# Kernel tuning notes

Hardware: AMD Instinct MI355X
Metric: run time of the kernel (lower is better)

## Reference

```python
import jax, jax.numpy as jnp
import numpy as np

B, G, IN, OUT, H, W = 8, 3, 384, 384, 64, 64
CG, OG = IN // G, OUT // G  # channels per group


def setup_inputs() -> dict:
    key = jax.random.key(0)
    ks = jax.random.split(key, 6)
    return {
        "input": jax.random.normal(ks[0], (B, IN, H, W), jnp.float32),
        "wh_pred": jax.random.uniform(ks[1], (B, 2 * G, H, W), jnp.float32),
        # conv_offset: 1x1 grouped conv, groups=G, in=2 per group, out=18 per group
        "w_off": jax.random.normal(ks[2], (G, 18, 2), jnp.float32) * 0.1,
        "b_off": jax.random.normal(ks[3], (G, 18), jnp.float32) * 0.1,
        # deformable 3x3 conv, groups=G: weight [OUT, IN/G, 3, 3]
        "w_d": jax.random.normal(ks[4], (OUT, CG, 3, 3), jnp.float32) * (1.0 / np.sqrt(CG * 9)),
        "b_d": jax.random.normal(ks[5], (OUT,), jnp.float32) * 0.01,
    }


def _bilinear_sample(img, py, px):
    # img: [Cg, H, W]; py, px: [9, H, W] float sampling positions
    # zero padding outside bounds (torchvision deform_conv2d semantics)
    y0 = jnp.floor(py)
    x0 = jnp.floor(px)
    wy = py - y0  # weight toward y0+1
    wx = px - x0
    y0i = y0.astype(jnp.int32)
    x0i = x0.astype(jnp.int32)

    def gather(yi, xi):
        valid = (yi >= 0) & (yi < H) & (xi >= 0) & (xi < W)
        yc = jnp.clip(yi, 0, H - 1)
        xc = jnp.clip(xi, 0, W - 1)
        v = img[:, yc, xc]  # [Cg, 9, H, W]
        return v * valid[None].astype(img.dtype)

    v00 = gather(y0i, x0i)
    v01 = gather(y0i, x0i + 1)
    v10 = gather(y0i + 1, x0i)
    v11 = gather(y0i + 1, x0i + 1)
    return (v00 * ((1 - wy) * (1 - wx))[None]
            + v01 * ((1 - wy) * wx)[None]
            + v10 * (wy * (1 - wx))[None]
            + v11 * (wy * wx)[None])  # [Cg, 9, H, W]


def _forward(input, wh_pred, w_off, b_off, w_d, b_d):
    # conv_offset: grouped 1x1 conv on detached wh_pred
    wh = jax.lax.stop_gradient(wh_pred).reshape(B, G, 2, H, W)
    off = jnp.einsum('bgchw,goc->bgohw', wh, w_off) + b_off[None, :, :, None, None]
    off = off.reshape(B, G, 9, 2, H, W)  # (dy, dx) per kernel tap

    # sampling positions for 3x3 kernel, stride 1, pad 1
    ky = (jnp.arange(9) // 3 - 1).astype(jnp.float32)
    kx = (jnp.arange(9) % 3 - 1).astype(jnp.float32)
    hh = jnp.arange(H, dtype=jnp.float32)
    ww = jnp.arange(W, dtype=jnp.float32)
    py = off[:, :, :, 0] + hh[None, None, None, :, None] + ky[None, None, :, None, None]
    px = off[:, :, :, 1] + ww[None, None, None, None, :] + kx[None, None, :, None, None]

    xg = input.reshape(B, G, CG, H, W)
    samp = jax.vmap(jax.vmap(_bilinear_sample))(xg, py, px)  # [B, G, Cg, 9, H, W]

    wg = w_d.reshape(G, OG, CG, 9)
    out = jnp.einsum('bgckhw,gock->bgohw', samp, wg)
    out = out.reshape(B, OUT, H, W) + b_d[None, :, None, None]
    return out


def reference(input, wh_pred, w_off, b_off, w_d, b_d):
    return _forward(input, wh_pred, w_off, b_off, w_d, b_d)
```

## Files before the change

kernel.cpp:

```cpp
#include <hip/hip_runtime.h>


typedef __attribute__((ext_vector_type(8))) short short8;
typedef __attribute__((ext_vector_type(4))) float floatx4;
typedef __attribute__((ext_vector_type(4))) unsigned int uintx4;

#define SLAB 524288
#define XT_GUARD 8704
#define XT_TAIL 512

__device__ __forceinline__ float bf_lo(unsigned int d) {
  return __uint_as_float(d << 16);
}
__device__ __forceinline__ float bf_hi(unsigned int d) {
  return __uint_as_float(d & 0xffff0000u);
}
__device__ __forceinline__ unsigned int cvtpk_bf16(float lo, float hi) {
  unsigned int r;
  asm("v_cvt_pk_bf16_f32 %0, %1, %2" : "=v"(r) : "v"(lo), "v"(hi));
  return r;
}

__global__ __launch_bounds__(256) void transpose_x_kernel(
    const float* __restrict__ in, ushort* __restrict__ xT) {
  __shared__ float tile[32][33];
  const int t  = threadIdx.x;
  const int tx = t & 31, ty = t >> 5;
  const int bx = blockIdx.x;
  const int x0 = (bx & 1) * 32;
  const int c0 = (bx >> 1) * 32;
  const int y  = blockIdx.y;
  const int bg = blockIdx.z;
  const int b  = bg / 3, g = bg % 3;

  const float* src = in + ((size_t)(b * 384 + g * 128)) * 4096 + (size_t)y * 64;
#pragma unroll
  for (int it = 0; it < 4; ++it) {
    int c = c0 + ty + it * 8;
    tile[ty + it * 8][tx] = src[(size_t)c * 4096 + x0 + tx];
  }
  __syncthreads();
  ushort* dst = xT + (((size_t)bg * 64 + y) * 64) * 128;
#pragma unroll
  for (int it = 0; it < 4; ++it) {
    int x = x0 + ty + it * 8;
    float v = tile[tx][ty + it * 8];
    dst[(size_t)x * 128 + c0 + tx] =
        (ushort)((__float_as_uint(v) + 0x8000u) >> 16);
  }
}

__global__ __launch_bounds__(256) void swizzle_w_kernel(
    const float* __restrict__ w_d, ushort* __restrict__ wB) {
  int idx = blockIdx.x * 256 + threadIdx.x;
  if (idx >= 442368) return;
  int j  = idx & 7;
  int l  = (idx >> 3) & 63;
  int f  = (idx >> 9) & 7;
  int s  = (idx >> 12) & 3;
  int t2 = idx >> 14;
  int k  = t2 % 9;
  int g  = t2 / 9;
  int o  = f * 16 + (l & 15);
  int c  = s * 32 + (l >> 4) * 8 + j;
  float v = w_d[((size_t)(g * 128 + o) * 128 + c) * 9 + k];
  wB[idx] = (ushort)((__float_as_uint(v) + 0x8000u) >> 16);
}

__global__ __launch_bounds__(256) void fa_main_mfma(
    const ushort* __restrict__ xT, const ushort* __restrict__ wB,
    const float* __restrict__ wh_pred, const float* __restrict__ w_off,
    const float* __restrict__ b_off, const float* __restrict__ b_d,
    float* __restrict__ out) {
  __shared__ int    off_s[9][32];
  __shared__ float4 w4_s[9][32];
  __shared__ ushort samp[32][128];

  const int t   = threadIdx.x;
  const int bid = blockIdx.x;
  const int b   = bid & 7;
  const int rem = bid >> 3;
  const int ph  = rem & 1;
  const int h   = (rem >> 1) & 63;
  const int g   = rem >> 7;
  const int pos0 = ph * 32;

  for (int idx = t; idx < 288; idx += 256) {
    int k = idx >> 5, pos = idx & 31;
    int posg = pos0 + pos;
    float wh0 = wh_pred[(((size_t)b * 6 + g * 2 + 0) * 64 + h) * 64 + posg];
    float wh1 = wh_pred[(((size_t)b * 6 + g * 2 + 1) * 64 + h) * 64 + posg];
    int oy_i = g * 18 + k * 2;
    int ox_i = oy_i + 1;
    float oy = fmaf(w_off[oy_i * 2], wh0, fmaf(w_off[oy_i * 2 + 1], wh1, b_off[oy_i]));
    float ox = fmaf(w_off[ox_i * 2], wh0, fmaf(w_off[ox_i * 2 + 1], wh1, b_off[ox_i]));
    float py = oy + (float)(h + k / 3 - 1);
    float px = ox + (float)(posg + k % 3 - 1);

    float fy = floorf(py), fx = floorf(px);
    int y0 = (int)fy, x0 = (int)fx;
    float wy = py - fy, wx = px - fx;
    float m_y0 = ((unsigned)y0 < 64u) ? 1.f : 0.f;
    float m_y1 = ((unsigned)(y0 + 1) < 64u) ? 1.f : 0.f;
    float m_x0 = ((unsigned)x0 < 64u) ? 1.f : 0.f;
    float m_x1 = ((unsigned)(x0 + 1) < 64u) ? 1.f : 0.f;
    float4 w4;
    w4.x = (1.f - wy) * (1.f - wx) * m_y0 * m_x0;
    w4.y = (1.f - wy) * wx * m_y0 * m_x1;
    w4.z = wy * (1.f - wx) * m_y1 * m_x0;
    w4.w = wy * wx * m_y1 * m_x1;
    int y0c = min(max(y0, -1), 63);
    int x0c = min(max(x0, -1), 63);
    off_s[k][pos] = (y0c * 64 + x0c) * 128;
    w4_s[k][pos]  = w4;
  }
  __syncthreads();

  const int wv  = t >> 6;
  const int l   = t & 63;
  const int l15 = l & 15;
  const int lhi = l >> 4;

  floatx4 acc[2][2];
#pragma unroll
  for (int ia = 0; ia < 2; ++ia) {
#pragma unroll
    for (int r = 0; r < 4; ++r) {
      float bias = b_d[g * 128 + wv * 32 + ia * 16 + lhi * 4 + r];
#pragma unroll
      for (int jb = 0; jb < 2; ++jb) acc[ia][jb][r] = bias;
    }
  }

  const int spos = t >> 3;
  const int scq  = t & 7;
  const int swz  = (spos & 7) << 3;
  const ushort* xb = xT + (size_t)(b * 3 + g) * SLAB;
  const ushort* wg = wB + (size_t)g * 9 * 16384;

  for (int k = 0; k < 9; ++k) {
    {
      int off   = off_s[k][spos];
      float4 w4 = w4_s[k][spos];
      const ushort* p00 = xb + off + scq * 16;
      const ushort* p10 = p00 + 8192;
#pragma unroll
      for (int j = 0; j < 2; ++j) {
        uintx4 a00 = *(const uintx4*)(p00 + j * 8);
        uintx4 a01 = *(const uintx4*)(p00 + j * 8 + 128);
        uintx4 a10 = *(const uintx4*)(p10 + j * 8);
        uintx4 a11 = *(const uintx4*)(p10 + j * 8 + 128);
        uintx4 pk;
#pragma unroll
        for (int d = 0; d < 4; ++d) {
          float lo = fmaf(bf_lo(a11[d]), w4.w, fmaf(bf_lo(a10[d]), w4.z,
                     fmaf(bf_lo(a01[d]), w4.y, bf_lo(a00[d]) * w4.x)));
          float hi = fmaf(bf_hi(a11[d]), w4.w, fmaf(bf_hi(a10[d]), w4.z,
                     fmaf(bf_hi(a01[d]), w4.y, bf_hi(a00[d]) * w4.x)));
          pk[d] = cvtpk_bf16(lo, hi);
        }
        *(uintx4*)&samp[spos][(scq * 16 + j * 8) ^ swz] = pk;
      }
    }
    __syncthreads();

    const ushort* wk = wg + (size_t)k * 16384;
#pragma unroll
    for (int s = 0; s < 4; ++s) {
      short8 a0 = *(const short8*)(wk + ((s * 8 + wv * 2 + 0) * 64 + l) * 8);
      short8 a1 = *(const short8*)(wk + ((s * 8 + wv * 2 + 1) * 64 + l) * 8);
      const int cb = (s * 32 + lhi * 8) ^ ((l15 & 7) << 3);
#pragma unroll
      for (int jb = 0; jb < 2; ++jb) {
        short8 bf = *(const short8*)&samp[jb * 16 + l15][cb];
        acc[0][jb] = __builtin_amdgcn_mfma_f32_16x16x32_bf16(a0, bf, acc[0][jb], 0, 0, 0);
        acc[1][jb] = __builtin_amdgcn_mfma_f32_16x16x32_bf16(a1, bf, acc[1][jb], 0, 0, 0);
      }
    }
    __syncthreads();
  }

#pragma unroll
  for (int ia = 0; ia < 2; ++ia) {
#pragma unroll
    for (int jb = 0; jb < 2; ++jb) {
#pragma unroll
      for (int r = 0; r < 4; ++r) {
        int o = wv * 32 + ia * 16 + lhi * 4 + r;
        int pos = pos0 + jb * 16 + l15;
        out[(((size_t)(b * 384 + g * 128 + o)) * 64 + h) * 64 + pos] = acc[ia][jb][r];
      }
    }
  }
}

extern "C" void kernel_launch(void* const* d_in, const int* in_sizes, int n_in,
                              void* d_out, int out_size, void* d_ws, size_t ws_size,
                              hipStream_t stream) {
  const float* input   = (const float*)d_in[0];
  const float* wh_pred = (const float*)d_in[1];
  const float* w_off   = (const float*)d_in[2];
  const float* b_off   = (const float*)d_in[3];
  const float* w_d     = (const float*)d_in[4];
  const float* b_d     = (const float*)d_in[5];
  float* out = (float*)d_out;

  ushort* xT = (ushort*)d_ws + XT_GUARD;
  ushort* wB = xT + (size_t)24 * SLAB + XT_TAIL;

  transpose_x_kernel<<<dim3(8, 64, 24), 256, 0, stream>>>(input, xT);
  swizzle_w_kernel<<<dim3(1728), 256, 0, stream>>>(w_d, wB);
  fa_main_mfma<<<dim3(3072), 256, 0, stream>>>(
      xT, wB, wh_pred, w_off, b_off, b_d, out);
}
```

Measured before the change: 87.51 us.

## Double-buffer sampled tile to overlap bilinear gather with MFMA

The sampled LDS tile is double-buffered, so the gather and interpolation for tap k+1 are issued before the MFMA work for tap k, with one barrier per tap instead of two. The thread-to-data mapping of the gather also changes: 16 lanes each load 8 channels of a position, across two positions per thread, giving contiguous 256-byte rows per 16-lane group. This is meant to hide global gather latency behind matrix work. In exchange it doubles the LDS used for samples and raises register pressure from loads held across the MFMA phase.

New measurement: 89.81 us. +2.6%, slower.

```diff
diff --git a/kernel.cpp b/kernel.cpp
--- a/kernel.cpp
+++ b/kernel.cpp
@@ -74,7 +74,7 @@
     float* __restrict__ out) {
   __shared__ int    off_s[9][32];
   __shared__ float4 w4_s[9][32];
-  __shared__ ushort samp[32][128];
+  __shared__ ushort samp[2][32][128];
 
   const int t   = threadIdx.x;
   const int bid = blockIdx.x;
@@ -132,38 +132,36 @@
     }
   }
 
-  const int spos = t >> 3;
-  const int scq  = t & 7;
-  const int swz  = (spos & 7) << 3;
+  const int spos16 = t >> 4;
+  const int lane16 = t & 15;
   const ushort* xb = xT + (size_t)(b * 3 + g) * SLAB;
   const ushort* wg = wB + (size_t)g * 9 * 16384;
 
-  for (int k = 0; k < 9; ++k) {
-    {
-      int off   = off_s[k][spos];
-      float4 w4 = w4_s[k][spos];
-      const ushort* p00 = xb + off + scq * 16;
-      const ushort* p10 = p00 + 8192;
-#pragma unroll
-      for (int j = 0; j < 2; ++j) {
-        uintx4 a00 = *(const uintx4*)(p00 + j * 8);
-        uintx4 a01 = *(const uintx4*)(p00 + j * 8 + 128);
-        uintx4 a10 = *(const uintx4*)(p10 + j * 8);
-        uintx4 a11 = *(const uintx4*)(p10 + j * 8 + 128);
-        uintx4 pk;
-#pragma unroll
-        for (int d = 0; d < 4; ++d) {
-          float lo = fmaf(bf_lo(a11[d]), w4.w, fmaf(bf_lo(a10[d]), w4.z,
-                     fmaf(bf_lo(a01[d]), w4.y, bf_lo(a00[d]) * w4.x)));
-          float hi = fmaf(bf_hi(a11[d]), w4.w, fmaf(bf_hi(a10[d]), w4.z,
-                     fmaf(bf_hi(a01[d]), w4.y, bf_hi(a00[d]) * w4.x)));
-          pk[d] = cvtpk_bf16(lo, hi);
-        }
-        *(uintx4*)&samp[spos][(scq * 16 + j * 8) ^ swz] = pk;
+  auto stage = [&](int k, ushort(*sb)[128]) {
+#pragma unroll
+    for (int p = 0; p < 2; ++p) {
+      int pos = p * 16 + spos16;
+      int off = off_s[k][pos];
+      float4 w4 = w4_s[k][pos];
+      const ushort* p00 = xb + off + lane16 * 8;
+      uintx4 a00 = *(const uintx4*)(p00);
+      uintx4 a01 = *(const uintx4*)(p00 + 128);
+      uintx4 a10 = *(const uintx4*)(p00 + 8192);
+      uintx4 a11 = *(const uintx4*)(p00 + 8320);
+      uintx4 pk;
+#pragma unroll
+      for (int d = 0; d < 4; ++d) {
+        float lo = fmaf(bf_lo(a11[d]), w4.w, fmaf(bf_lo(a10[d]), w4.z,
+                   fmaf(bf_lo(a01[d]), w4.y, bf_lo(a00[d]) * w4.x)));
+        float hi = fmaf(bf_hi(a11[d]), w4.w, fmaf(bf_hi(a10[d]), w4.z,
+                   fmaf(bf_hi(a01[d]), w4.y, bf_hi(a00[d]) * w4.x)));
+        pk[d] = cvtpk_bf16(lo, hi);
       }
-    }
-    __syncthreads();
-
+      *(uintx4*)&sb[pos][(lane16 * 8) ^ ((pos & 7) << 3)] = pk;
+    }
+  };
+
+  auto mfma_phase = [&](int k, const ushort(*sb)[128]) {
     const ushort* wk = wg + (size_t)k * 16384;
 #pragma unroll
     for (int s = 0; s < 4; ++s) {
@@ -172,11 +170,18 @@
       const int cb = (s * 32 + lhi * 8) ^ ((l15 & 7) << 3);
 #pragma unroll
       for (int jb = 0; jb < 2; ++jb) {
-        short8 bf = *(const short8*)&samp[jb * 16 + l15][cb];
+        short8 bf = *(const short8*)&sb[jb * 16 + l15][cb];
         acc[0][jb] = __builtin_amdgcn_mfma_f32_16x16x32_bf16(a0, bf, acc[0][jb], 0, 0, 0);
         acc[1][jb] = __builtin_amdgcn_mfma_f32_16x16x32_bf16(a1, bf, acc[1][jb], 0, 0, 0);
       }
     }
+  };
+
+  stage(0, samp[0]);
+  __syncthreads();
+  for (int k = 0; k < 9; ++k) {
+    if (k < 8) stage(k + 1, samp[(k + 1) & 1]);
+    mfma_phase(k, samp[k & 1]);
     __syncthreads();
   }
 
```
